# Kernel tuning notes

Measured on AMD Instinct MI355X. Metric: run time of the kernel, lower is better.

## Reference

```python
import jax, jax.numpy as jnp
import numpy as np

N = 8192
E = 262144
D_IN = 256
D_OUT = 256
EPS = 1e-05


def setup_inputs() -> dict:
    key = jax.random.key(0)
    kx, ke0, ke1, kw = jax.random.split(key, 4)
    x = jax.random.normal(kx, (N, D_IN), dtype=jnp.float32)
    edge_index = jnp.stack([
        jax.random.randint(ke0, (E,), 0, N, dtype=jnp.int64),
        jax.random.randint(ke1, (E,), 0, N, dtype=jnp.int64),
    ], axis=0)
    # nn.Linear(in, out, bias=False): weight shape [out, in], kaiming-uniform-ish init
    bound = 1.0 / np.sqrt(D_IN)
    W = jax.random.uniform(kw, (D_OUT, D_IN), dtype=jnp.float32, minval=-bound, maxval=bound)
    return {"x": x, "edge_index": edge_index, "W": W}


def reference(x, edge_index, W):
    n = x.shape[0]
    # A_hat = I with edges set to 1 (set semantics; duplicates harmless)
    A_hat = jnp.eye(n, dtype=x.dtype).at[edge_index[0], edge_index[1]].set(1.0)
    # D_hat = diag(1/sqrt(rowsum + eps)); A_norm = D_hat @ A_hat @ D_hat
    d_inv = 1.0 / jnp.sqrt(A_hat.sum(axis=1) + EPS)  # [N]
    A_norm = d_inv[:, None] * A_hat * d_inv[None, :]  # [N, N]
    h = x @ W.T  # [N, D_OUT]
    return jax.nn.relu(A_norm @ h)
```

## Files before the change

kernel.cpp:

```cpp
#include <hip/hip_runtime.h>
#include <hip/hip_bf16.h>
#include <math.h>

#define N_NODES 8192
#define DIM 256
#define WPR 256
#define LSTRIDE 128

typedef __attribute__((ext_vector_type(8))) short bf16x8;
typedef __attribute__((ext_vector_type(4))) float f32x4;

__global__ __launch_bounds__(256) void k1_convert_scatter(
        const float* __restrict__ x, const float* __restrict__ W, const int* __restrict__ ei,
        __hip_bfloat16* __restrict__ xb, __hip_bfloat16* __restrict__ Wb,
        unsigned short* __restrict__ list, int* __restrict__ lens, int E) {
    const int CONV_BLOCKS = (N_NODES * DIM / 8 + DIM * DIM / 8) / 256;
    if ((int)blockIdx.x < CONV_BLOCKS) {
        int t = blockIdx.x * 256 + threadIdx.x;
        const int NX8 = N_NODES * DIM / 8;
        const float* src = x;
        __hip_bfloat16* dst = xb;
        size_t off = (size_t)t * 8;
        if (t >= NX8) { src = W; dst = Wb; off = (size_t)(t - NX8) * 8; }
        float4 v0 = *(const float4*)(src + off);
        float4 v1 = *(const float4*)(src + off + 4);
        union { __hip_bfloat16 h[8]; uint4 u; } c;
        c.h[0] = __float2bfloat16(v0.x); c.h[1] = __float2bfloat16(v0.y);
        c.h[2] = __float2bfloat16(v0.z); c.h[3] = __float2bfloat16(v0.w);
        c.h[4] = __float2bfloat16(v1.x); c.h[5] = __float2bfloat16(v1.y);
        c.h[6] = __float2bfloat16(v1.z); c.h[7] = __float2bfloat16(v1.w);
        *(uint4*)(dst + off) = c.u;
    } else {
        int sid = (blockIdx.x - CONV_BLOCKS) * 256 + threadIdx.x;
        int snth = (gridDim.x - CONV_BLOCKS) * 256;
        const int* rows = ei;
        const int* cols = ei + E;
        for (int e = sid; e < E; e += snth) {
            int r = rows[e];
            int c = cols[e];
            int pos = atomicAdd(&lens[r], 1);
            if (pos < LSTRIDE) list[(size_t)r * LSTRIDE + pos] = (unsigned short)c;
        }
    }
}

__global__ __launch_bounds__(256) void k2_gemm_dedup(
        const short* __restrict__ xb, const short* __restrict__ Wb, __hip_bfloat16* __restrict__ g,
        unsigned short* __restrict__ list, int* __restrict__ lens, float* __restrict__ dinv) {
    __shared__ unsigned sbm[4][WPR];
    if ((int)blockIdx.x < 512) {
        int tid = threadIdx.x;
        int wave = tid >> 6, lane = tid & 63;
        int quad = lane >> 4, l16 = lane & 15;
        int t = blockIdx.x;
        int bm = (t & 127) * 64 + wave * 16;
        int bn = (t >> 7) * 64;
        f32x4 acc[4] = {};
        const short* arow = xb + (size_t)(bm + l16) * DIM + quad * 8;
#pragma unroll
        for (int k0 = 0; k0 < DIM; k0 += 32) {
            bf16x8 a = *(const bf16x8*)(arow + k0);
#pragma unroll
            for (int s = 0; s < 4; s++) {
                bf16x8 b = *(const bf16x8*)(Wb + (size_t)(bn + s * 16 + l16) * DIM + k0 + quad * 8);
                acc[s] = __builtin_amdgcn_mfma_f32_16x16x32_bf16(a, b, acc[s], 0, 0, 0);
            }
        }
#pragma unroll
        for (int r = 0; r < 4; r++) {
            int m = bm + quad * 4 + r;
#pragma unroll
            for (int s = 0; s < 4; s++)
                g[(size_t)m * DIM + bn + s * 16 + l16] = __float2bfloat16(acc[s][r]);
        }
    } else {
        int bid = blockIdx.x - 512;
        int wave = threadIdx.x >> 6, lane = threadIdx.x & 63;
        for (int row = bid * 4 + wave; row < N_NODES; row += 512 * 4) {
            uint4 z = {0u, 0u, 0u, 0u};
            *(uint4*)&sbm[wave][lane * 4] = z;
            unsigned short* lp = list + (size_t)row * LSTRIDE;
            int raw = lens[row];
            if (raw > LSTRIDE) raw = LSTRIDE;
            int c0 = (lane < raw) ? (int)lp[lane] : -1;
            int c1 = (64 + lane < raw) ? (int)lp[64 + lane] : -1;
            int new0 = 0, new1 = 0;
            if (c0 >= 0) {
                unsigned old = atomicOr(&sbm[wave][c0 >> 5], 1u << (c0 & 31));
                new0 = !((old >> (c0 & 31)) & 1u);
            }
            if (c1 >= 0) {
                unsigned old = atomicOr(&sbm[wave][c1 >> 5], 1u << (c1 & 31));
                new1 = !((old >> (c1 & 31)) & 1u);
            }
            unsigned long long m0 = __ballot(new0);
            unsigned long long m1 = __ballot(new1);
            unsigned long long below = (1ull << lane) - 1ull;
            int kept0 = __popcll(m0);
            int pos0 = __popcll(m0 & below);
            int pos1 = kept0 + __popcll(m1 & below);
            int total = kept0 + __popcll(m1);
            int diag = (int)((sbm[wave][row >> 5] >> (row & 31)) & 1u);
            if (new0) lp[pos0] = (unsigned short)c0;
            if (new1) lp[pos1] = (unsigned short)c1;
            if (!diag && lane == 0) lp[total] = (unsigned short)row;
            if (lane == 0) {
                int len = total + (diag ? 0 : 1);
                lens[row] = len;
                dinv[row] = 1.0f / sqrtf((float)len + 1e-5f);
            }
        }
    }
}

__global__ __launch_bounds__(128) void k3_aggregate(
        const unsigned short* __restrict__ list, const int* __restrict__ lens,
        const float* __restrict__ dinv, const uint4* __restrict__ g4, float* __restrict__ out) {
    __shared__ unsigned short snbr[LSTRIDE];
    __shared__ float sdj[LSTRIDE];
    __shared__ float part[4][DIM];
    int row = blockIdx.x;
    int tid = threadIdx.x;
    unsigned short nb = list[(size_t)row * LSTRIDE + tid];
    snbr[tid] = nb;
    sdj[tid] = dinv[nb & (N_NODES - 1)];
    int len = lens[row];
    __syncthreads();
    int gq = tid >> 5, l = tid & 31;
    float a0 = 0.f, a1 = 0.f, a2 = 0.f, a3 = 0.f, a4 = 0.f, a5 = 0.f, a6 = 0.f, a7 = 0.f;
    float b0 = 0.f, b1 = 0.f, b2 = 0.f, b3 = 0.f, b4 = 0.f, b5 = 0.f, b6 = 0.f, b7 = 0.f;
    int i = gq;
    for (; i + 4 < len; i += 8) {
        int n0 = snbr[i];
        int n1 = snbr[i + 4];
        float d0 = sdj[i];
        float d1 = sdj[i + 4];
        uint4 u0 = g4[(size_t)n0 * 32 + l];
        uint4 u1 = g4[(size_t)n1 * 32 + l];
        a0 = fmaf(d0, __uint_as_float(u0.x << 16), a0);
        a1 = fmaf(d0, __uint_as_float(u0.x & 0xffff0000u), a1);
        a2 = fmaf(d0, __uint_as_float(u0.y << 16), a2);
        a3 = fmaf(d0, __uint_as_float(u0.y & 0xffff0000u), a3);
        a4 = fmaf(d0, __uint_as_float(u0.z << 16), a4);
        a5 = fmaf(d0, __uint_as_float(u0.z & 0xffff0000u), a5);
        a6 = fmaf(d0, __uint_as_float(u0.w << 16), a6);
        a7 = fmaf(d0, __uint_as_float(u0.w & 0xffff0000u), a7);
        b0 = fmaf(d1, __uint_as_float(u1.x << 16), b0);
        b1 = fmaf(d1, __uint_as_float(u1.x & 0xffff0000u), b1);
        b2 = fmaf(d1, __uint_as_float(u1.y << 16), b2);
        b3 = fmaf(d1, __uint_as_float(u1.y & 0xffff0000u), b3);
        b4 = fmaf(d1, __uint_as_float(u1.z << 16), b4);
        b5 = fmaf(d1, __uint_as_float(u1.z & 0xffff0000u), b5);
        b6 = fmaf(d1, __uint_as_float(u1.w << 16), b6);
        b7 = fmaf(d1, __uint_as_float(u1.w & 0xffff0000u), b7);
    }
    if (i < len) {
        int n0 = snbr[i];
        float d0 = sdj[i];
        uint4 u0 = g4[(size_t)n0 * 32 + l];
        a0 = fmaf(d0, __uint_as_float(u0.x << 16), a0);
        a1 = fmaf(d0, __uint_as_float(u0.x & 0xffff0000u), a1);
        a2 = fmaf(d0, __uint_as_float(u0.y << 16), a2);
        a3 = fmaf(d0, __uint_as_float(u0.y & 0xffff0000u), a3);
        a4 = fmaf(d0, __uint_as_float(u0.z << 16), a4);
        a5 = fmaf(d0, __uint_as_float(u0.z & 0xffff0000u), a5);
        a6 = fmaf(d0, __uint_as_float(u0.w << 16), a6);
        a7 = fmaf(d0, __uint_as_float(u0.w & 0xffff0000u), a7);
    }
    float* pp = &part[gq][l * 8];
    pp[0] = a0 + b0; pp[1] = a1 + b1; pp[2] = a2 + b2; pp[3] = a3 + b3;
    pp[4] = a4 + b4; pp[5] = a5 + b5; pp[6] = a6 + b6; pp[7] = a7 + b7;
    __syncthreads();
    int f0 = tid * 2;
    float s = dinv[row];
    float r0 = (part[0][f0] + part[1][f0]) + (part[2][f0] + part[3][f0]);
    float r1 = (part[0][f0 + 1] + part[1][f0 + 1]) + (part[2][f0 + 1] + part[3][f0 + 1]);
    float2 o;
    o.x = fmaxf(s * r0, 0.f);
    o.y = fmaxf(s * r1, 0.f);
    *(float2*)(out + (size_t)row * DIM + f0) = o;
}

extern "C" void kernel_launch(void* const* d_in, const int* in_sizes, int n_in,
                              void* d_out, int out_size, void* d_ws, size_t ws_size,
                              hipStream_t stream) {
    const float* x = (const float*)d_in[0];
    const int* ei = (const int*)d_in[1];
    const float* W = (const float*)d_in[2];
    float* out = (float*)d_out;
    int E = in_sizes[1] / 2;

    unsigned char* ws = (unsigned char*)d_ws;
    size_t off = 0;
    int* lens = (int*)(ws + off);                       off += (size_t)N_NODES * 4;
    float* dinv = (float*)(ws + off);                   off += (size_t)N_NODES * 4;
    unsigned short* list = (unsigned short*)(ws + off); off += (size_t)N_NODES * LSTRIDE * 2;
    __hip_bfloat16* xb = (__hip_bfloat16*)(ws + off);   off += (size_t)N_NODES * DIM * 2;
    __hip_bfloat16* Wb = (__hip_bfloat16*)(ws + off);   off += (size_t)DIM * DIM * 2;
    __hip_bfloat16* g = (__hip_bfloat16*)(ws + off);    off += (size_t)N_NODES * DIM * 2;

    hipMemsetAsync(lens, 0, (size_t)N_NODES * 4, stream);
    const int CONV_BLOCKS = (N_NODES * DIM / 8 + DIM * DIM / 8) / 256;
    k1_convert_scatter<<<CONV_BLOCKS + 512, 256, 0, stream>>>(x, W, ei, xb, Wb, list, lens, E);
    k2_gemm_dedup<<<1024, 256, 0, stream>>>((const short*)xb, (const short*)Wb, g, list, lens, dinv);
    k3_aggregate<<<N_NODES, 128, 0, stream>>>(list, lens, dinv, (const uint4*)g, out);
}
```

Baseline: 103.2 us.

## Fuse x bf16 conversion into GEMM loads and replace memset with prep kernel

```diff
diff --git a/kernel.cpp b/kernel.cpp
--- a/kernel.cpp
+++ b/kernel.cpp
@@ -10,42 +10,45 @@
 typedef __attribute__((ext_vector_type(8))) short bf16x8;
 typedef __attribute__((ext_vector_type(4))) float f32x4;
 
-__global__ __launch_bounds__(256) void k1_convert_scatter(
-        const float* __restrict__ x, const float* __restrict__ W, const int* __restrict__ ei,
-        __hip_bfloat16* __restrict__ xb, __hip_bfloat16* __restrict__ Wb,
-        unsigned short* __restrict__ list, int* __restrict__ lens, int E) {
-    const int CONV_BLOCKS = (N_NODES * DIM / 8 + DIM * DIM / 8) / 256;
-    if ((int)blockIdx.x < CONV_BLOCKS) {
-        int t = blockIdx.x * 256 + threadIdx.x;
-        const int NX8 = N_NODES * DIM / 8;
-        const float* src = x;
-        __hip_bfloat16* dst = xb;
-        size_t off = (size_t)t * 8;
-        if (t >= NX8) { src = W; dst = Wb; off = (size_t)(t - NX8) * 8; }
-        float4 v0 = *(const float4*)(src + off);
-        float4 v1 = *(const float4*)(src + off + 4);
+__global__ __launch_bounds__(256) void p0_prep(const float* __restrict__ W,
+                                               __hip_bfloat16* __restrict__ Wb,
+                                               int* __restrict__ lens) {
+    int t = blockIdx.x * 256 + threadIdx.x;
+    if (t < N_NODES / 4) {
+        uint4 z = {0u, 0u, 0u, 0u};
+        ((uint4*)lens)[t] = z;
+    }
+    int w = t - N_NODES / 4;
+    if (w >= 0 && w < DIM * DIM / 8) {
+        size_t off = (size_t)w * 8;
+        float4 v0 = *(const float4*)(W + off);
+        float4 v1 = *(const float4*)(W + off + 4);
         union { __hip_bfloat16 h[8]; uint4 u; } c;
         c.h[0] = __float2bfloat16(v0.x); c.h[1] = __float2bfloat16(v0.y);
         c.h[2] = __float2bfloat16(v0.z); c.h[3] = __float2bfloat16(v0.w);
         c.h[4] = __float2bfloat16(v1.x); c.h[5] = __float2bfloat16(v1.y);
         c.h[6] = __float2bfloat16(v1.z); c.h[7] = __float2bfloat16(v1.w);
-        *(uint4*)(dst + off) = c.u;
-    } else {
-        int sid = (blockIdx.x - CONV_BLOCKS) * 256 + threadIdx.x;
-        int snth = (gridDim.x - CONV_BLOCKS) * 256;
-        const int* rows = ei;
-        const int* cols = ei + E;
-        for (int e = sid; e < E; e += snth) {
-            int r = rows[e];
-            int c = cols[e];
-            int pos = atomicAdd(&lens[r], 1);
-            if (pos < LSTRIDE) list[(size_t)r * LSTRIDE + pos] = (unsigned short)c;
-        }
+        *(uint4*)(Wb + off) = c.u;
+    }
+}
+
+__global__ __launch_bounds__(256) void k1_scatter(const int* __restrict__ ei,
+                                                  unsigned short* __restrict__ list,
+                                                  int* __restrict__ lens, int E) {
+    int sid = blockIdx.x * 256 + threadIdx.x;
+    int snth = gridDim.x * 256;
+    const int* rows = ei;
+    const int* cols = ei + E;
+    for (int e = sid; e < E; e += snth) {
+        int r = rows[e];
+        int c = cols[e];
+        int pos = atomicAdd(&lens[r], 1);
+        if (pos < LSTRIDE) list[(size_t)r * LSTRIDE + pos] = (unsigned short)c;
     }
 }
 
 __global__ __launch_bounds__(256) void k2_gemm_dedup(
-        const short* __restrict__ xb, const short* __restrict__ Wb, __hip_bfloat16* __restrict__ g,
+        const float* __restrict__ x, const short* __restrict__ Wb, __hip_bfloat16* __restrict__ g,
         unsigned short* __restrict__ list, int* __restrict__ lens, float* __restrict__ dinv) {
     __shared__ unsigned sbm[4][WPR];
     if ((int)blockIdx.x < 512) {
@@ -56,14 +59,20 @@
         int bm = (t & 127) * 64 + wave * 16;
         int bn = (t >> 7) * 64;
         f32x4 acc[4] = {};
-        const short* arow = xb + (size_t)(bm + l16) * DIM + quad * 8;
+        const float* arow = x + (size_t)(bm + l16) * DIM + quad * 8;
 #pragma unroll
         for (int k0 = 0; k0 < DIM; k0 += 32) {
-            bf16x8 a = *(const bf16x8*)(arow + k0);
+            float4 v0 = *(const float4*)(arow + k0);
+            float4 v1 = *(const float4*)(arow + k0 + 4);
+            union { __hip_bfloat16 h[8]; bf16x8 v; } ac;
+            ac.h[0] = __float2bfloat16(v0.x); ac.h[1] = __float2bfloat16(v0.y);
+            ac.h[2] = __float2bfloat16(v0.z); ac.h[3] = __float2bfloat16(v0.w);
+            ac.h[4] = __float2bfloat16(v1.x); ac.h[5] = __float2bfloat16(v1.y);
+            ac.h[6] = __float2bfloat16(v1.z); ac.h[7] = __float2bfloat16(v1.w);
 #pragma unroll
             for (int s = 0; s < 4; s++) {
                 bf16x8 b = *(const bf16x8*)(Wb + (size_t)(bn + s * 16 + l16) * DIM + k0 + quad * 8);
-                acc[s] = __builtin_amdgcn_mfma_f32_16x16x32_bf16(a, b, acc[s], 0, 0, 0);
+                acc[s] = __builtin_amdgcn_mfma_f32_16x16x32_bf16(ac.v, b, acc[s], 0, 0, 0);
             }
         }
 #pragma unroll
@@ -121,10 +130,12 @@
     __shared__ float part[4][DIM];
     int row = blockIdx.x;
     int tid = threadIdx.x;
-    unsigned short nb = list[(size_t)row * LSTRIDE + tid];
-    snbr[tid] = nb;
-    sdj[tid] = dinv[nb & (N_NODES - 1)];
     int len = lens[row];
+    if (tid < len) {
+        unsigned short nb = list[(size_t)row * LSTRIDE + tid];
+        snbr[tid] = nb;
+        sdj[tid] = dinv[nb];
+    }
     __syncthreads();
     int gq = tid >> 5, l = tid & 31;
     float a0 = 0.f, a1 = 0.f, a2 = 0.f, a3 = 0.f, a4 = 0.f, a5 = 0.f, a6 = 0.f, a7 = 0.f;
@@ -195,13 +206,12 @@
     int* lens = (int*)(ws + off);                       off += (size_t)N_NODES * 4;
     float* dinv = (float*)(ws + off);                   off += (size_t)N_NODES * 4;
     unsigned short* list = (unsigned short*)(ws + off); off += (size_t)N_NODES * LSTRIDE * 2;
-    __hip_bfloat16* xb = (__hip_bfloat16*)(ws + off);   off += (size_t)N_NODES * DIM * 2;
     __hip_bfloat16* Wb = (__hip_bfloat16*)(ws + off);   off += (size_t)DIM * DIM * 2;
     __hip_bfloat16* g = (__hip_bfloat16*)(ws + off);    off += (size_t)N_NODES * DIM * 2;
 
-    hipMemsetAsync(lens, 0, (size_t)N_NODES * 4, stream);
-    const int CONV_BLOCKS = (N_NODES * DIM / 8 + DIM * DIM / 8) / 256;
-    k1_convert_scatter<<<CONV_BLOCKS + 512, 256, 0, stream>>>(x, W, ei, xb, Wb, list, lens, E);
-    k2_gemm_dedup<<<1024, 256, 0, stream>>>((const short*)xb, (const short*)Wb, g, list, lens, dinv);
+    const int P0_THREADS = N_NODES / 4 + DIM * DIM / 8;
+    p0_prep<<<(P0_THREADS + 255) / 256, 256, 0, stream>>>(W, Wb, lens);
+    k1_scatter<<<512, 256, 0, stream>>>(ei, list, lens, E);
+    k2_gemm_dedup<<<1024, 256, 0, stream>>>(x, (const short*)Wb, g, list, lens, dinv);
     k3_aggregate<<<N_NODES, 128, 0, stream>>>(list, lens, dinv, (const uint4*)g, out);
 }
```

Result: no change. 103.8 us (+0.6%).
